# Optimization experiments

Measured on AMD Instinct MI355X. Metric: run time of the kernel, lower is better.

## Reference

```python
import jax, jax.numpy as jnp
import numpy as np

SZ = 256          # image side
K = 4             # neighbors
NUM_CHANNELS = 8
CHUNK = 512       # query chunk for brute-force KNN
BIG = 1e10        # penalty added to squared distance of non-filled candidates


def _fill_channel(img, mask):
    """img: [SZ,SZ] float, mask: [SZ,SZ] bool. Returns filled [SZ,SZ].

    Faithful to TreeMultiRandom: filled pixels = mask nonzero; for every
    unfilled pixel take K nearest filled pixels (Euclidean on coords/SZ,
    i.e. norm_coord) and fill with sum(val_j * dist_j) / sum(dist_j)
    (NOTE: the original weights by distance, not inverse distance; kept as-is).
    Filled pixels keep their (masked) value.
    """
    N = SZ * SZ
    r = jnp.arange(SZ, dtype=jnp.float32) / SZ  # norm_coord
    gy, gx = jnp.meshgrid(r, r, indexing='ij')  # (row, col) like .nonzero()
    py = gy.reshape(N)
    px = gx.reshape(N)
    mflat = mask.reshape(N)
    vflat = (img * mask).reshape(N)  # holed image values
    penalty = jnp.where(mflat, 0.0, BIG).astype(jnp.float32)

    def chunk_fn(q):
        qy, qx = q  # each [CHUNK]
        # masked squared distances to all candidates: [CHUNK, N]
        d2 = (qy[:, None] - py[None, :]) ** 2 + (qx[:, None] - px[None, :]) ** 2 \
             + penalty[None, :]
        neg, idx = jax.lax.top_k(-d2, K)          # K smallest distances
        dist = jnp.sqrt(jnp.maximum(-neg, 0.0))   # [CHUNK, K] (KDTree returns L2)
        v = vflat[idx]                            # gather neighbor values
        return jnp.sum(v * dist, axis=1) / jnp.sum(dist, axis=1)

    qys = py.reshape(-1, CHUNK)
    qxs = px.reshape(-1, CHUNK)
    vals = jax.lax.map(chunk_fn, (qys, qxs)).reshape(N)
    # unfilled pixels get interpolated vals; filled keep holed value
    return jnp.where(mflat, vflat, vals).reshape(SZ, SZ)


def reference(coded, lookup_table):
    img = coded[0, 0]  # [SZ, SZ]
    chans = [_fill_channel(img, lookup_table == c)
             for c in range(1, NUM_CHANNELS + 1)]
    return jnp.stack(chans)[None]  # [1, NUM_CHANNELS, SZ, SZ]


def setup_inputs() -> dict:
    key = jax.random.key(0)
    k1, k2 = jax.random.split(key)
    coded = jax.random.normal(k1, (1, 1, SZ, SZ), dtype=jnp.float32)
    # values in 1..NUM_CHANNELS so every channel has a nonempty filled set
    lookup_table = jax.random.randint(k2, (SZ, SZ), 1, NUM_CHANNELS + 1,
                                      dtype=jnp.int32)
    return {"coded": coded, "lookup_table": lookup_table}
```

## Files before the change

kernel.cpp:

```cpp
#include <hip/hip_runtime.h>
#include <math.h>

#define SZ 256
#define KNN 4
#define NUM_CHANNELS 8
#define R 7
#define WROWS (2 * R + 1)
#define RSTRIDE 6

typedef unsigned long long u64;

__device__ __forceinline__ void insert_key(u64 key, u64& k0, u64& k1,
                                           u64& k2, u64& k3) {
    if (key < k3) {
        u64 mx;
        mx = (k2 > key) ? k2 : key;  k3 = (k3 < mx) ? k3 : mx;
        mx = (k1 > key) ? k1 : key;  k2 = (k2 < mx) ? k2 : mx;
        mx = (k0 > key) ? k0 : key;  k1 = (k1 < mx) ? k1 : mx;
        k0 = (k0 < key) ? k0 : key;
    }
}

__global__ __launch_bounds__(256) void build_bitmaps(
    const int* __restrict__ lut,
    u64* __restrict__ bm)
{
    const int y = blockIdx.x;
    const int x = threadIdx.x;
    const int v = lut[y * SZ + x];
    const int lane = threadIdx.x & 63;
    const int w64 = x >> 6;
    #pragma unroll
    for (int c = 1; c <= NUM_CHANNELS; ++c) {
        u64 bal = __ballot(v == c);
        if (lane == 0) bm[(size_t)(c - 1) * (SZ * 4) + y * 4 + w64] = bal;
    }
}

__global__ __launch_bounds__(256) void knn_fill(
    const float* __restrict__ img,
    const u64* __restrict__ bm,
    float* __restrict__ out)
{
    __shared__ u64 win[WROWS * RSTRIDE];

    const int x = threadIdx.x;
    const int y = blockIdx.x;
    const int ch = blockIdx.y;
    const u64* bmc = bm + (size_t)ch * (SZ * 4);

    for (int i = threadIdx.x; i < WROWS * RSTRIDE; i += 256) {
        const int rr = i / RSTRIDE, j = i - rr * RSTRIDE;
        const int yy = y - R + rr;
        u64 v = 0;
        if (j >= 1 && j <= 4 && yy >= 0 && yy < SZ) v = bmc[yy * 4 + (j - 1)];
        win[i] = v;
    }
    __syncthreads();

    const int pix = y * SZ + x;
    float* outc = out + (size_t)ch * (SZ * SZ);

    const bool is_filled =
        (win[R * RSTRIDE + 1 + (x >> 6)] >> (x & 63)) & 1ull;
    if (is_filled) {
        outc[pix] = img[pix];
        return;
    }

    u64 k0 = ~0ull, k1 = ~0ull, k2 = ~0ull, k3 = ~0ull;

    const int base = x - R + 64;
    const int wrd = base >> 6;
    const int sh  = base & 63;

    #pragma unroll
    for (int rr = 0; rr < WROWS; ++rr) {
        const u64 lo = win[rr * RSTRIDE + wrd];
        const u64 hi = win[rr * RSTRIDE + wrd + 1];
        u64 w = (u64)(((((unsigned __int128)hi) << 64) | lo) >> sh)
                & ((1u << WROWS) - 1);
        const int dy = rr - R;
        const int dy2 = dy * dy;
        const int rowbase = (y + dy) * SZ;
        while (w) {
            const int b = __builtin_ctzll(w);
            w &= w - 1;
            const int dx = b - R;
            const u64 d2 = (u64)(dy2 + dx * dx);
            const u64 key = (d2 << 16) | (unsigned)(rowbase + x + dx);
            insert_key(key, k0, k1, k2, k3);
        }
    }

    if ((k3 >> 16) >= (u64)((R + 1) * (R + 1))) {
        k0 = k1 = k2 = k3 = ~0ull;
        for (int ady = 0; ady < SZ; ++ady) {
            const u64 cur = k3 >> 16;
            const u64 a2 = (u64)(ady * ady);
            if (a2 > cur) break;
            int Rx;
            const u64 bound = cur - a2;
            if (bound >= 65025ull) Rx = SZ - 1;
            else Rx = (int)sqrtf((float)bound) + 1;
            int xs = x - Rx; if (xs < 0) xs = 0;
            int xe = x + Rx; if (xe > SZ - 1) xe = SZ - 1;
            const int jxs = xs >> 6, jxe = xe >> 6;
            const u64 mlo = (~0ull) << (xs & 63);
            const u64 mhi = (~0ull) >> (63 - (xe & 63));
            for (int s = 0; s < 2; ++s) {
                if (s && ady == 0) continue;
                const int yy = s ? y + ady : y - ady;
                if (yy < 0 || yy > SZ - 1) continue;
                const int rb = yy * SZ;
                for (int j = jxs; j <= jxe; ++j) {
                    u64 w = bmc[yy * 4 + j];
                    if (j == jxs) w &= mlo;
                    if (j == jxe) w &= mhi;
                    while (w) {
                        const int b = __builtin_ctzll(w);
                        w &= w - 1;
                        const int xx = (j << 6) + b;
                        const int dxx = xx - x;
                        const u64 d2 = a2 + (u64)(dxx * dxx);
                        insert_key((d2 << 16) | (unsigned)(rb + xx),
                                   k0, k1, k2, k3);
                    }
                }
            }
        }
    }

    u64 ks[KNN] = { k0, k1, k2, k3 };
    float num = 0.0f, den = 0.0f;
    #pragma unroll
    for (int i = 0; i < KNN; ++i) {
        const int idx = (int)(ks[i] & 0xFFFFull);
        const int d2i = (int)(ks[i] >> 16);
        const float dist = sqrtf((float)d2i * (1.0f / 65536.0f));
        num += img[idx] * dist;
        den += dist;
    }
    outc[pix] = num / den;
}

extern "C" void kernel_launch(void* const* d_in, const int* in_sizes, int n_in,
                              void* d_out, int out_size, void* d_ws, size_t ws_size,
                              hipStream_t stream) {
    const float* img = (const float*)d_in[0];
    const int*   lut = (const int*)d_in[1];
    float*       out = (float*)d_out;
    u64*         bm  = (u64*)d_ws;

    build_bitmaps<<<dim3(SZ), dim3(256), 0, stream>>>(lut, bm);
    knn_fill<<<dim3(SZ, NUM_CHANNELS), dim3(256), 0, stream>>>(img, bm, out);
}
```

Measured before the change: 86.52 us.

## Fuse bitmap construction into KNN kernel and use 32-bit top-4 keys

Removes the separate bitmap-building kernel: each block ballots the lookup table rows of its window directly into shared memory, which saves one launch and a workspace round trip. The local window search now packs squared distance and pixel index into 32-bit keys and does a branchless 4-way insert, and the window radius shrinks from 7 to 6. The rare fallback global search now scans lookup-table entries directly instead of bitmap words. The trade-offs are that each of the 8 channel blocks re-reads up to 13 rows of the lookup table, and the fallback path becomes a per-pixel scan that will run more often with the smaller window.

```diff
diff --git a/kernel.cpp b/kernel.cpp
--- a/kernel.cpp
+++ b/kernel.cpp
@@ -4,100 +4,100 @@
 #define SZ 256
 #define KNN 4
 #define NUM_CHANNELS 8
-#define R 7
+#define R 6
 #define WROWS (2 * R + 1)
 #define RSTRIDE 6
 
 typedef unsigned long long u64;
+typedef unsigned int u32;
 
-__device__ __forceinline__ void insert_key(u64 key, u64& k0, u64& k1,
-                                           u64& k2, u64& k3) {
-    if (key < k3) {
-        u64 mx;
-        mx = (k2 > key) ? k2 : key;  k3 = (k3 < mx) ? k3 : mx;
-        mx = (k1 > key) ? k1 : key;  k2 = (k2 < mx) ? k2 : mx;
-        mx = (k0 > key) ? k0 : key;  k1 = (k1 < mx) ? k1 : mx;
-        k0 = (k0 < key) ? k0 : key;
-    }
+__device__ __forceinline__ void ins4(u32 key, u32& k0, u32& k1,
+                                     u32& k2, u32& k3) {
+    u32 m;
+    m = (k2 > key) ? k2 : key;  k3 = (k3 < m) ? k3 : m;
+    m = (k1 > key) ? k1 : key;  k2 = (k2 < m) ? k2 : m;
+    m = (k0 > key) ? k0 : key;  k1 = (k1 < m) ? k1 : m;
+    k0 = (k0 < key) ? k0 : key;
 }
 
-__global__ __launch_bounds__(256) void build_bitmaps(
-    const int* __restrict__ lut,
-    u64* __restrict__ bm)
-{
-    const int y = blockIdx.x;
-    const int x = threadIdx.x;
-    const int v = lut[y * SZ + x];
-    const int lane = threadIdx.x & 63;
-    const int w64 = x >> 6;
-    #pragma unroll
-    for (int c = 1; c <= NUM_CHANNELS; ++c) {
-        u64 bal = __ballot(v == c);
-        if (lane == 0) bm[(size_t)(c - 1) * (SZ * 4) + y * 4 + w64] = bal;
+__device__ __forceinline__ void ins4_64(u64 key, u64& k0, u64& k1,
+                                        u64& k2, u64& k3) {
+    if (key < k3) {
+        u64 m;
+        m = (k2 > key) ? k2 : key;  k3 = (k3 < m) ? k3 : m;
+        m = (k1 > key) ? k1 : key;  k2 = (k2 < m) ? k2 : m;
+        m = (k0 > key) ? k0 : key;  k1 = (k1 < m) ? k1 : m;
+        k0 = (k0 < key) ? k0 : key;
     }
 }
 
 __global__ __launch_bounds__(256) void knn_fill(
     const float* __restrict__ img,
-    const u64* __restrict__ bm,
-    float* __restrict__ out)
+    const int*   __restrict__ lut,
+    float*       __restrict__ out)
 {
     __shared__ u64 win[WROWS * RSTRIDE];
 
-    const int x = threadIdx.x;
-    const int y = blockIdx.x;
-    const int ch = blockIdx.y;
-    const u64* bmc = bm + (size_t)ch * (SZ * 4);
+    const int x    = threadIdx.x;
+    const int y    = blockIdx.x;
+    const int ch   = blockIdx.y;
+    const int c    = ch + 1;
+    const int lane = x & 63;
+    const int w64  = x >> 6;
 
-    for (int i = threadIdx.x; i < WROWS * RSTRIDE; i += 256) {
-        const int rr = i / RSTRIDE, j = i - rr * RSTRIDE;
+    if (threadIdx.x < WROWS * RSTRIDE) win[threadIdx.x] = 0;
+    __syncthreads();
+    #pragma unroll
+    for (int rr = 0; rr < WROWS; ++rr) {
         const int yy = y - R + rr;
-        u64 v = 0;
-        if (j >= 1 && j <= 4 && yy >= 0 && yy < SZ) v = bmc[yy * 4 + (j - 1)];
-        win[i] = v;
+        int v = 0;
+        if (yy >= 0 && yy < SZ) v = lut[yy * SZ + x];
+        const u64 bal = __ballot(v == c);
+        if (lane == 0) win[rr * RSTRIDE + 1 + w64] = bal;
     }
     __syncthreads();
 
     const int pix = y * SZ + x;
     float* outc = out + (size_t)ch * (SZ * SZ);
 
-    const bool is_filled =
-        (win[R * RSTRIDE + 1 + (x >> 6)] >> (x & 63)) & 1ull;
-    if (is_filled) {
+    if ((win[R * RSTRIDE + 1 + (x >> 6)] >> (x & 63)) & 1ull) {
         outc[pix] = img[pix];
         return;
     }
 
-    u64 k0 = ~0ull, k1 = ~0ull, k2 = ~0ull, k3 = ~0ull;
+    u32 k0 = ~0u, k1 = ~0u, k2 = ~0u, k3 = ~0u;
 
     const int base = x - R + 64;
-    const int wrd = base >> 6;
-    const int sh  = base & 63;
+    const int wrd  = base >> 6;
+    const int sh   = base & 63;
 
     #pragma unroll
     for (int rr = 0; rr < WROWS; ++rr) {
         const u64 lo = win[rr * RSTRIDE + wrd];
         const u64 hi = win[rr * RSTRIDE + wrd + 1];
-        u64 w = (u64)(((((unsigned __int128)hi) << 64) | lo) >> sh)
+        u32 w = (u32)((u64)(((((unsigned __int128)hi) << 64) | lo) >> sh))
                 & ((1u << WROWS) - 1);
-        const int dy = rr - R;
+        const int dy  = rr - R;
         const int dy2 = dy * dy;
-        const int rowbase = (y + dy) * SZ;
+        const int rowx = (y + dy) * SZ + x;
         while (w) {
-            const int b = __builtin_ctzll(w);
+            const int b = __builtin_ctz(w);
             w &= w - 1;
-            const int dx = b - R;
-            const u64 d2 = (u64)(dy2 + dx * dx);
-            const u64 key = (d2 << 16) | (unsigned)(rowbase + x + dx);
-            insert_key(key, k0, k1, k2, k3);
+            const int dx  = b - R;
+            const u32 d2  = (u32)(dy2 + dx * dx);
+            const u32 key = (d2 << 16) | (u32)(rowx + dx);
+            ins4(key, k0, k1, k2, k3);
         }
     }
 
-    if ((k3 >> 16) >= (u64)((R + 1) * (R + 1))) {
-        k0 = k1 = k2 = k3 = ~0ull;
+    u64 ks[KNN];
+    if ((k3 >> 16) < (u32)((R + 1) * (R + 1))) {
+        ks[0] = k0; ks[1] = k1; ks[2] = k2; ks[3] = k3;
+    } else {
+        u64 q0 = ~0ull, q1 = ~0ull, q2 = ~0ull, q3 = ~0ull;
         for (int ady = 0; ady < SZ; ++ady) {
-            const u64 cur = k3 >> 16;
-            const u64 a2 = (u64)(ady * ady);
+            const u64 cur = q3 >> 16;
+            const u64 a2  = (u64)(ady * ady);
             if (a2 > cur) break;
             int Rx;
             const u64 bound = cur - a2;
@@ -105,33 +105,23 @@
             else Rx = (int)sqrtf((float)bound) + 1;
             int xs = x - Rx; if (xs < 0) xs = 0;
             int xe = x + Rx; if (xe > SZ - 1) xe = SZ - 1;
-            const int jxs = xs >> 6, jxe = xe >> 6;
-            const u64 mlo = (~0ull) << (xs & 63);
-            const u64 mhi = (~0ull) >> (63 - (xe & 63));
             for (int s = 0; s < 2; ++s) {
                 if (s && ady == 0) continue;
                 const int yy = s ? y + ady : y - ady;
                 if (yy < 0 || yy > SZ - 1) continue;
                 const int rb = yy * SZ;
-                for (int j = jxs; j <= jxe; ++j) {
-                    u64 w = bmc[yy * 4 + j];
-                    if (j == jxs) w &= mlo;
-                    if (j == jxe) w &= mhi;
-                    while (w) {
-                        const int b = __builtin_ctzll(w);
-                        w &= w - 1;
-                        const int xx = (j << 6) + b;
+                for (int xx = xs; xx <= xe; ++xx) {
+                    if (lut[rb + xx] == c) {
                         const int dxx = xx - x;
                         const u64 d2 = a2 + (u64)(dxx * dxx);
-                        insert_key((d2 << 16) | (unsigned)(rb + xx),
-                                   k0, k1, k2, k3);
+                        ins4_64((d2 << 16) | (u32)(rb + xx), q0, q1, q2, q3);
                     }
                 }
             }
         }
+        ks[0] = q0; ks[1] = q1; ks[2] = q2; ks[3] = q3;
     }
 
-    u64 ks[KNN] = { k0, k1, k2, k3 };
     float num = 0.0f, den = 0.0f;
     #pragma unroll
     for (int i = 0; i < KNN; ++i) {
@@ -150,8 +140,6 @@
     const float* img = (const float*)d_in[0];
     const int*   lut = (const int*)d_in[1];
     float*       out = (float*)d_out;
-    u64*         bm  = (u64*)d_ws;
 
-    build_bitmaps<<<dim3(SZ), dim3(256), 0, stream>>>(lut, bm);
-    knn_fill<<<dim3(SZ, NUM_CHANNELS), dim3(256), 0, stream>>>(img, bm, out);
+    knn_fill<<<dim3(SZ, NUM_CHANNELS), dim3(256), 0, stream>>>(img, lut, out);
 }
```

Measured after the change: 122.7 us. 41.9% more time.
